# Performance work log

Measured on AMD Instinct MI355X. Metric: run time of the kernel, lower is better.

Reference implementation:

```python
import jax, jax.numpy as jnp
import numpy as np

# dims
B, C, H, W = 8, 256, 64, 128
P = 4                      # patch size (p1 == p2)
E = C // 2                 # embed dim = ngf//2 = Mamba d_model
HP, WP = H // P, W // P
N = HP * WP                # 512 tokens
DM = E                     # Mamba d_model
DI = 2 * DM                # d_inner (expand=2)
DS = 16                    # d_state
DC = 4                     # d_conv
DR = DM // 16              # dt_rank
NG = 128                   # new_ngf
S = 2                      # pixel-shuffle stride


def setup_inputs() -> dict:
    key = jax.random.key(0)
    ks = jax.random.split(key, 16)
    g = lambda i, shape, s=0.02: jax.random.normal(ks[i], shape, jnp.float32) * s
    return {
        'x': jax.random.normal(ks[0], (B, C, H, W), jnp.float32),
        # patch embed (conv k=stride=P)
        'patch_w': g(1, (E, C, P, P)),
        'patch_b': jnp.zeros((E,), jnp.float32),
        # Mamba params
        'in_proj_w': g(2, (2 * DI, DM)),
        'conv1d_w': g(3, (DI, DC), 0.1),
        'conv1d_b': jnp.zeros((DI,), jnp.float32),
        'x_proj_w': g(4, (DR + 2 * DS, DI)),
        'dt_proj_w': g(5, (DI, DR), 0.1),
        'dt_proj_b': jnp.full((DI,), -3.0, jnp.float32),
        'A_log': jnp.log(jnp.broadcast_to(jnp.arange(1, DS + 1, dtype=jnp.float32), (DI, DS))),
        'D_param': jnp.ones((DI,), jnp.float32),
        'out_proj_w': g(6, (DM, DI)),
        # unpatchify linear N -> N*P*P
        'lin_w': g(7, (N * P * P, N)),
        'lin_b': jnp.zeros((N * P * P,), jnp.float32),
        # nerv conv (3x3, out = new_ngf*S*S)
        'conv_w': g(8, (NG * S * S, E, 3, 3), 0.05),
        'conv_b': jnp.zeros((NG * S * S,), jnp.float32),
        # residual FFN (1x1)
        'ffn_w1': g(9, (NG, NG)),
        'ffn_b1': jnp.zeros((NG,), jnp.float32),
        'ffn_w2': g(10, (NG, NG)),
        'ffn_b2': jnp.zeros((NG,), jnp.float32),
    }


def reference(x, patch_w, patch_b, in_proj_w, conv1d_w, conv1d_b, x_proj_w,
              dt_proj_w, dt_proj_b, A_log, D_param, out_proj_w, lin_w, lin_b,
              conv_w, conv_b, ffn_w1, ffn_b1, ffn_w2, ffn_b2):
    silu = jax.nn.silu
    # ---- patch embed: (B,C,H,W) -> (B,N,E)
    t = jax.lax.conv_general_dilated(x, patch_w, (P, P), 'VALID',
                                     dimension_numbers=('NCHW', 'OIHW', 'NCHW'))
    t = t + patch_b[None, :, None, None]
    t = t.reshape(B, E, N).transpose(0, 2, 1)  # (B,N,E)

    # ---- Mamba selective scan
    xz = jnp.einsum('bld,ed->ble', t, in_proj_w)      # (B,N,2*DI)
    xin, z = jnp.split(xz, 2, axis=-1)
    # depthwise causal conv1d over sequence
    xp = jnp.pad(xin, ((0, 0), (DC - 1, 0), (0, 0)))
    xc = sum(xp[:, k:k + N, :] * conv1d_w[:, k] for k in range(DC)) + conv1d_b
    xc = silu(xc)                                     # (B,N,DI)
    dbl = jnp.einsum('bld,ed->ble', xc, x_proj_w)
    dt, Bs, Cs = dbl[..., :DR], dbl[..., DR:DR + DS], dbl[..., DR + DS:]
    dt = jax.nn.softplus(jnp.einsum('blr,dr->bld', dt, dt_proj_w) + dt_proj_b)
    A = -jnp.exp(A_log)                               # (DI,DS)
    dA = jnp.exp(dt[..., None] * A)                   # (B,N,DI,DS)
    dBx = dt[..., None] * Bs[:, :, None, :] * xc[..., None]

    def step(h, inputs):
        dA_t, dBx_t, C_t = inputs
        h = dA_t * h + dBx_t                          # (B,DI,DS)
        y = jnp.einsum('bdn,bn->bd', h, C_t)
        return h, y

    h0 = jnp.zeros((B, DI, DS), xc.dtype)
    _, ys = jax.lax.scan(step, h0, (dA.transpose(1, 0, 2, 3),
                                    dBx.transpose(1, 0, 2, 3),
                                    Cs.transpose(1, 0, 2)))
    y = ys.transpose(1, 0, 2) + D_param * xc
    y = y * silu(z)
    out = jnp.einsum('bld,ed->ble', y, out_proj_w)    # (B,N,DM)

    # ---- unpatchify: (B,N,E) -> (B,E,H,W)
    u = out.transpose(0, 2, 1)                        # (B,E,N)
    u = jnp.einsum('ben,mn->bem', u, lin_w) + lin_b   # (B,E,N*P*P)
    u = u.reshape(B, E, HP, WP, P, P).transpose(0, 1, 2, 4, 3, 5)
    u = u.reshape(B, E, H, W)

    # ---- nerv block: 3x3 conv -> pixel shuffle -> gelu
    c = jax.lax.conv_general_dilated(u, conv_w, (1, 1), ((1, 1), (1, 1)),
                                     dimension_numbers=('NCHW', 'OIHW', 'NCHW'))
    c = c + conv_b[None, :, None, None]               # (B,NG*S*S,H,W)
    c = c.reshape(B, NG, S, S, H, W).transpose(0, 1, 4, 2, 5, 3)
    c = c.reshape(B, NG, H * S, W * S)
    c = jax.nn.gelu(c)

    # ---- residual FFN (1x1 convs over channels)
    f = jax.nn.gelu(jnp.einsum('bchw,ec->behw', c, ffn_w1) + ffn_b1[None, :, None, None])
    f = jnp.einsum('behw,ce->bchw', f, ffn_w2) + ffn_b2[None, :, None, None]
    return c + f
```

## Files before the change

### kernel.cpp

```cpp
#include <hip/hip_runtime.h>
#include <hip/hip_bf16.h>

#define HW2 32768

typedef __attribute__((ext_vector_type(8))) short short8v;
typedef __attribute__((ext_vector_type(4))) float f32x4;

__device__ __forceinline__ float siluf(float x){ return x / (1.f + __expf(-x)); }
__device__ __forceinline__ float geluf(float v){
  float t = 0.7978845608028654f * fmaf(0.044715f*v*v, v, v);
  t = fminf(fmaxf(t, -15.f), 15.f);
  float e = __expf(2.f*t);
  return 0.5f*v*(1.f + (e-1.f)/(e+1.f));
}
__device__ __forceinline__ ushort bf16rne(float f){
  unsigned u = __float_as_uint(f);
  unsigned r = (u + 0x7fffu + ((u >> 16) & 1u)) >> 16;
  return (ushort)r;
}
__device__ __forceinline__ float bf2f(ushort u){ return __uint_as_float(((unsigned)u) << 16); }
__device__ __forceinline__ void split2(float v, ushort& h, ushort& lo){
  h = bf16rne(v);
  lo = bf16rne(v - bf2f(h));
}

__global__ __launch_bounds__(256) void k_prep(uint4* __restrict__ ubf4,
                                              const float* __restrict__ cw, ushort* __restrict__ wbf,
                                              const float* __restrict__ w1, const float* __restrict__ w2,
                                              ushort* __restrict__ wpad,
                                              const float* __restrict__ lw, ushort* __restrict__ lwbf){
  int bid = blockIdx.x;
  int tid = threadIdx.x;
  if (bid < 32) {
    uint4 z = make_uint4(0,0,0,0);
    size_t base4 = (size_t)bid * 34320;
    for (int i = tid; i < 1552; i += 256) {
      size_t off;
      if (i < 520)       off = i;
      else if (i < 1040) off = 33800 + (i - 520);
      else {
        int j = i - 1040;
        int row = 1 + (j >> 3);
        int colsel = (j >> 2) & 1, q = j & 3;
        off = (size_t)row*520 + colsel*516 + q;
      }
      ubf4[base4 + off] = z;
    }
  } else if (bid < 2336) {
    int idx = (bid - 32)*256 + tid;
    int j    = idx & 7;
    int lane = (idx >> 3) & 63;
    int f    = (idx >> 9) & 3;
    int tap  = (idx >> 11) % 9;
    int rest = idx / 18432;
    int ec = rest & 3, ocg = rest >> 2;
    int o = ocg*64 + f*16 + (lane & 15);
    int e = ec*32 + (lane >> 4)*8 + j;
    wbf[idx] = bf16rne(cw[((size_t)o*128 + e)*9 + tap]);
  } else if (bid < 2472) {
    int idx = (bid - 2336)*256 + tid;
    int which = idx / 17408;
    int rem = idx - which*17408;
    int e = rem / 136, k = rem - e*136;
    const float* s = which ? w2 : w1;
    wpad[idx] = (k < 128) ? bf16rne(s[e*128 + k]) : (ushort)0;
  } else {
    int i = (bid - 2472)*256 + tid;
    float4 v = reinterpret_cast<const float4*>(lw)[i];
    uint2 u;
    u.x = (uint)bf16rne(v.x) | ((uint)bf16rne(v.y) << 16);
    u.y = (uint)bf16rne(v.z) | ((uint)bf16rne(v.w) << 16);
    reinterpret_cast<uint2*>(lwbf)[i] = u;
  }
}

__global__ __launch_bounds__(256) void k_ytr(const float* __restrict__ yo, ushort* __restrict__ ybfT){
  __shared__ float tile[32][132];
  int b = blockIdx.x, n0 = blockIdx.y*32;
  int tid = threadIdx.x;
  for (int it = 0; it < 16; ++it) {
    int idx = it*256 + tid;
    int row = idx >> 7, e = idx & 127;
    tile[row][e] = yo[((size_t)(b*512 + n0 + row))*128 + e];
  }
  __syncthreads();
  int e = tid >> 1, half = tid & 1;
  uint* dst = reinterpret_cast<uint*>(ybfT + ((size_t)b*128 + e)*512 + n0 + half*16);
  #pragma unroll
  for (int j = 0; j < 8; ++j) {
    int n = half*16 + j*2;
    dst[j] = (uint)bf16rne(tile[n][e]) | ((uint)bf16rne(tile[n+1][e]) << 16);
  }
}

__global__ __launch_bounds__(256) void k_patchm(const float* __restrict__ x, const float* __restrict__ pw,
                                                float* __restrict__ part){
  __shared__ ushort Ah[4096], Al[4096], Wh[4096], Wl[4096];
  int m0 = blockIdx.x * 128;
  int ks = blockIdx.y;
  int tid = threadIdx.x;
  int l = tid & 63, wv = tid >> 6;
  int wm = wv >> 1, we = wv & 1;
  int lj = l & 15, lg = l >> 4;
  f32x4 acc[4][4];
  #pragma unroll
  for (int a = 0; a < 4; ++a)
    #pragma unroll
    for (int b = 0; b < 4; ++b)
      acc[a][b] = (f32x4){0.f,0.f,0.f,0.f};
  int kbase = ks * 256;

  for (int it = 0; it < 8; ++it) {
    int k0 = kbase + it*32;
    __syncthreads();
    #pragma unroll
    for (int q = 0; q < 4; ++q) {
      int flat = q*256 + tid;
      int row = flat & 127, kk4 = flat >> 7;
      int m = m0 + row;
      int bb = m >> 9, ll = m & 511;
      int hp = ll >> 5, wp = ll & 31;
      int k = k0 + kk4*4;
      int c = k >> 4, i2 = (k >> 2) & 3;
      float4 v = *reinterpret_cast<const float4*>(x + (((bb*256 + c)*64 + hp*4 + i2)*128 + wp*4));
      ushort h0,h1,h2,h3,q0,q1,q2,q3;
      split2(v.x,h0,q0); split2(v.y,h1,q1); split2(v.z,h2,q2); split2(v.w,h3,q3);
      uint2 uh, ul;
      uh.x = (uint)h0 | ((uint)h1 << 16); uh.y = (uint)h2 | ((uint)h3 << 16);
      ul.x = (uint)q0 | ((uint)q1 << 16); ul.y = (uint)q2 | ((uint)q3 << 16);
      int lane = ((kk4 >> 1) << 4) | (row & 15);
      int dst = ((row >> 4)*64 + lane)*8 + (kk4 & 1)*4;
      *reinterpret_cast<uint2*>(Ah + dst) = uh;
      *reinterpret_cast<uint2*>(Al + dst) = ul;
    }
    #pragma unroll
    for (int q = 0; q < 4; ++q) {
      int flat = q*256 + tid;
      int e = flat >> 3, kk4 = flat & 7;
      float4 v = *reinterpret_cast<const float4*>(pw + (size_t)e*4096 + k0 + kk4*4);
      ushort h0,h1,h2,h3,q0,q1,q2,q3;
      split2(v.x,h0,q0); split2(v.y,h1,q1); split2(v.z,h2,q2); split2(v.w,h3,q3);
      uint2 uh, ul;
      uh.x = (uint)h0 | ((uint)h1 << 16); uh.y = (uint)h2 | ((uint)h3 << 16);
      ul.x = (uint)q0 | ((uint)q1 << 16); ul.y = (uint)q2 | ((uint)q3 << 16);
      int lane = ((kk4 >> 1) << 4) | (e & 15);
      int dst = ((e >> 4)*64 + lane)*8 + (kk4 & 1)*4;
      *reinterpret_cast<uint2*>(Wh + dst) = uh;
      *reinterpret_cast<uint2*>(Wl + dst) = ul;
    }
    __syncthreads();

    short8v ah[4], al_[4], wh[4], wl_[4];
    #pragma unroll
    for (int f = 0; f < 4; ++f) {
      ah[f]  = *reinterpret_cast<const short8v*>(Ah + ((wm*4 + f)*64 + l)*8);
      al_[f] = *reinterpret_cast<const short8v*>(Al + ((wm*4 + f)*64 + l)*8);
      wh[f]  = *reinterpret_cast<const short8v*>(Wh + ((we*4 + f)*64 + l)*8);
      wl_[f] = *reinterpret_cast<const short8v*>(Wl + ((we*4 + f)*64 + l)*8);
    }
    #pragma unroll
    for (int fo = 0; fo < 4; ++fo)
      #pragma unroll
      for (int fj = 0; fj < 4; ++fj) {
        acc[fo][fj] = __builtin_amdgcn_mfma_f32_16x16x32_bf16(ah[fo],  wh[fj],  acc[fo][fj], 0, 0, 0);
        acc[fo][fj] = __builtin_amdgcn_mfma_f32_16x16x32_bf16(ah[fo],  wl_[fj], acc[fo][fj], 0, 0, 0);
        acc[fo][fj] = __builtin_amdgcn_mfma_f32_16x16x32_bf16(al_[fo], wh[fj],  acc[fo][fj], 0, 0, 0);
      }
  }
  float* pb = part + (size_t)ks*524288;
  #pragma unroll
  for (int fo = 0; fo < 4; ++fo) {
    int m = m0 + wm*64 + fo*16 + lg*4;
    #pragma unroll
    for (int fj = 0; fj < 4; ++fj) {
      int e = we*64 + fj*16 + lj;
      f32x4 a = acc[fo][fj];
      pb[(size_t)(m+0)*128 + e] = a.x;
      pb[(size_t)(m+1)*128 + e] = a.y;
      pb[(size_t)(m+2)*128 + e] = a.z;
      pb[(size_t)(m+3)*128 + e] = a.w;
    }
  }
}

__global__ __launch_bounds__(256) void k_tred(const float* __restrict__ part, const float* __restrict__ pb,
                                              float* __restrict__ t){
  int i = blockIdx.x*256 + threadIdx.x;
  const float4* p4 = reinterpret_cast<const float4*>(part);
  float4 s = reinterpret_cast<const float4*>(pb)[i & 31];
  #pragma unroll
  for (int ks = 0; ks < 16; ++ks) {
    float4 v = p4[(size_t)ks*131072 + i];
    s.x += v.x; s.y += v.y; s.z += v.z; s.w += v.w;
  }
  reinterpret_cast<float4*>(t)[i] = s;
}

__global__ __launch_bounds__(256) void k_gemm(const float* __restrict__ A, const float* __restrict__ W,
                                              float* __restrict__ C, int M, int N, int K){
  __shared__ __align__(16) float As[16][68];
  __shared__ __align__(16) float Bs[16][68];
  int m0 = blockIdx.x * 64, n0 = blockIdx.y * 64;
  int tid = threadIdx.x;
  int tm = tid >> 4, tn = tid & 15;
  int lm = tid >> 2, kq = tid & 3;
  float acc[4][4] = {};
  const float* Abase = A + (size_t)(m0 + lm)*K + kq*4;
  const float* Wbase = W + (size_t)(n0 + lm)*K + kq*4;
  for (int k0 = 0; k0 < K; k0 += 16) {
    float4 av = *reinterpret_cast<const float4*>(Abase + k0);
    float4 bv = *reinterpret_cast<const float4*>(Wbase + k0);
    As[kq*4+0][lm]=av.x; As[kq*4+1][lm]=av.y; As[kq*4+2][lm]=av.z; As[kq*4+3][lm]=av.w;
    Bs[kq*4+0][lm]=bv.x; Bs[kq*4+1][lm]=bv.y; Bs[kq*4+2][lm]=bv.z; Bs[kq*4+3][lm]=bv.w;
    __syncthreads();
    #pragma unroll
    for (int kk = 0; kk < 16; ++kk) {
      float4 a = *reinterpret_cast<const float4*>(&As[kk][tm*4]);
      float4 b = *reinterpret_cast<const float4*>(&Bs[kk][tn*4]);
      float ar[4] = {a.x,a.y,a.z,a.w};
      float br[4] = {b.x,b.y,b.z,b.w};
      #pragma unroll
      for (int i = 0; i < 4; ++i)
        #pragma unroll
        for (int j = 0; j < 4; ++j)
          acc[i][j] = fmaf(ar[i], br[j], acc[i][j]);
    }
    __syncthreads();
  }
  #pragma unroll
  for (int i = 0; i < 4; ++i) {
    float4 ov = make_float4(acc[i][0], acc[i][1], acc[i][2], acc[i][3]);
    *reinterpret_cast<float4*>(C + (size_t)(m0 + tm*4 + i)*N + n0 + tn*4) = ov;
  }
}

__global__ __launch_bounds__(256) void k_conv1d(const float* __restrict__ xz, const float* __restrict__ w,
                                                const float* __restrict__ bias, float* __restrict__ xc){
  int idx = blockIdx.x*256 + threadIdx.x;
  int d = idx & 255;
  int l = (idx >> 8) & 511;
  int bb = idx >> 17;
  const float* base = xz + (size_t)bb*512*512 + d;
  float s = bias[d];
  #pragma unroll
  for (int k = 0; k < 4; ++k) {
    int ls = l - 3 + k;
    if (ls >= 0) s = fmaf(base[(size_t)ls*512], w[d*4+k], s);
  }
  xc[idx] = s / (1.f + __expf(-s));
}

__global__ __launch_bounds__(256) void k_xproj(const float* __restrict__ xc, const float* __restrict__ xpw,
                                               const float* __restrict__ dtw, const float* __restrict__ dtb,
                                               float* __restrict__ dbl, float* __restrict__ dt){
  __shared__ __align__(16) float sxc[256];
  __shared__ float sdbl[40];
  int bl = blockIdx.x;
  int tid = threadIdx.x;
  sxc[tid] = xc[(size_t)bl*256 + tid];
  __syncthreads();
  if (tid < 160) {
    int g = tid >> 2, kq = tid & 3;
    const float4* wr = reinterpret_cast<const float4*>(xpw + g*256) + kq;
    const float4* xr = reinterpret_cast<const float4*>(sxc) + kq;
    float s = 0.f;
    #pragma unroll
    for (int i = 0; i < 16; ++i) {
      float4 w = wr[i*4], xv = xr[i*4];
      s += w.x*xv.x + w.y*xv.y + w.z*xv.z + w.w*xv.w;
    }
    s += __shfl_xor(s, 1);
    s += __shfl_xor(s, 2);
    if (kq == 0) {
      sdbl[g] = s;
      dbl[(size_t)bl*40 + g] = s;
    }
  }
  __syncthreads();
  float s = dtb[tid];
  const float* wr = dtw + tid*8;
  #pragma unroll
  for (int r = 0; r < 8; ++r) s = fmaf(sdbl[r], wr[r], s);
  float sp = (s > 20.f) ? s : log1pf(__expf(s));
  dt[(size_t)bl*256 + tid] = sp;
}

__global__ __launch_bounds__(256) void k_scanA(const float* __restrict__ dt, const float* __restrict__ dbl,
                                               const float* __restrict__ xc, const float* __restrict__ A_log,
                                               float* __restrict__ aprod, float* __restrict__ hend){
  __shared__ float sdt[32][16], sxc[32][16], sB[32][16];
  int tid = threadIdx.x;
  int bg = blockIdx.x;
  int ch = blockIdx.y;
  int bb = bg >> 4, dgrp = bg & 15;
  int l0 = ch*32;
  #pragma unroll
  for (int it = 0; it < 2; ++it) {
    int idx = it*256 + tid;
    int t = idx >> 4, dd = idx & 15;
    int base = bb*512 + l0 + t;
    sdt[t][dd] = dt[(size_t)base*256 + dgrp*16 + dd];
    sxc[t][dd] = xc[(size_t)base*256 + dgrp*16 + dd];
    sB [t][dd] = dbl[(size_t)base*40 + 8 + dd];
  }
  __syncthreads();
  int n = tid & 15, dloc = tid >> 4;
  float Ac = -__expf(A_log[(dgrp*16 + dloc)*16 + n]);
  float a = 1.f, h = 0.f;
  #pragma unroll
  for (int t = 0; t < 32; ++t) {
    float dtv = sdt[t][dloc], xcv = sxc[t][dloc], Bv = sB[t][n];
    float dA = __expf(dtv*Ac);
    h = fmaf(dA, h, dtv*Bv*xcv);
    a *= dA;
  }
  aprod[(size_t)(bg*16 + ch)*256 + tid] = a;
  hend [(size_t)(bg*16 + ch)*256 + tid] = h;
}

__global__ __launch_bounds__(256) void k_scanC(const float* __restrict__ dt, const float* __restrict__ dbl,
                                               const float* __restrict__ xc, const float* __restrict__ xz,
                                               const float* __restrict__ A_log, const float* __restrict__ Dp,
                                               const float* __restrict__ aprod, const float* __restrict__ hend,
                                               float* __restrict__ y){
  __shared__ float sdt[32][16], sxc[32][16], sB[32][16], sC[32][16], sz[32][16];
  int tid = threadIdx.x;
  int bg = blockIdx.x;
  int ch = blockIdx.y;
  int bb = bg >> 4, dgrp = bg & 15;
  int l0 = ch*32;
  #pragma unroll
  for (int it = 0; it < 2; ++it) {
    int idx = it*256 + tid;
    int t = idx >> 4, dd = idx & 15;
    int base = bb*512 + l0 + t;
    sdt[t][dd] = dt[(size_t)base*256 + dgrp*16 + dd];
    sxc[t][dd] = xc[(size_t)base*256 + dgrp*16 + dd];
    sB [t][dd] = dbl[(size_t)base*40 + 8  + dd];
    sC [t][dd] = dbl[(size_t)base*40 + 24 + dd];
    sz [t][dd] = xz[(size_t)base*512 + 256 + dgrp*16 + dd];
  }
  float h = 0.f;
  for (int cc = 0; cc < ch; ++cc) {
    size_t idx = (size_t)(bg*16 + cc)*256 + tid;
    h = fmaf(aprod[idx], h, hend[idx]);
  }
  __syncthreads();
  int n = tid & 15, dloc = tid >> 4;
  int d = dgrp*16 + dloc;
  float Ac = -__expf(A_log[d*16 + n]);
  float Dv = Dp[d];
  #pragma unroll 4
  for (int t = 0; t < 32; ++t) {
    float dtv = sdt[t][dloc], xcv = sxc[t][dloc];
    float Bv = sB[t][n], Cv = sC[t][n];
    float dA = __expf(dtv*Ac);
    h = fmaf(dA, h, dtv*Bv*xcv);
    float yp = h*Cv;
    yp += __shfl_xor(yp, 1, 16);
    yp += __shfl_xor(yp, 2, 16);
    yp += __shfl_xor(yp, 4, 16);
    yp += __shfl_xor(yp, 8, 16);
    if (n == 0) {
      float zv = sz[t][dloc];
      y[(size_t)(bb*512 + l0 + t)*256 + d] = (yp + Dv*xcv) * (zv / (1.f + __expf(-zv)));
    }
  }
}

__global__ __launch_bounds__(512) void k_linm(const ushort* __restrict__ ybfT, const ushort* __restrict__ lwbf,
                                              const float* __restrict__ lb, ushort* __restrict__ ubf){
  __shared__ ushort As[128*88];
  __shared__ ushort Bs[128*88];
  int m0 = blockIdx.x * 128;
  int b  = blockIdx.y;
  int tid = threadIdx.x;
  int l = tid & 63, wv = tid >> 6;
  int wm = wv & 3, we = wv >> 2;
  int lj = l & 15, lg = l >> 4;
  f32x4 acc[4][2];
  #pragma unroll
  for (int fo = 0; fo < 4; ++fo)
    #pragma unroll
    for (int fj = 0; fj < 2; ++fj)
      acc[fo][fj] = (f32x4){0.f,0.f,0.f,0.f};

  for (int k0 = 0; k0 < 512; k0 += 64) {
    __syncthreads();
    #pragma unroll
    for (int it = 0; it < 2; ++it) {
      int flat = it*512 + tid;
      int e = flat >> 3, kc8 = flat & 7;
      *reinterpret_cast<uint4*>(&As[e*88 + kc8*8]) =
        *reinterpret_cast<const uint4*>(ybfT + ((size_t)b*128 + e)*512 + k0 + kc8*8);
      *reinterpret_cast<uint4*>(&Bs[e*88 + kc8*8]) =
        *reinterpret_cast<const uint4*>(lwbf + (size_t)(m0 + e)*512 + k0 + kc8*8);
    }
    __syncthreads();
    #pragma unroll
    for (int kc = 0; kc < 2; ++kc) {
      short8v af[4], bq[2];
      #pragma unroll
      for (int fo = 0; fo < 4; ++fo)
        af[fo] = *reinterpret_cast<const short8v*>(&As[(we*64 + fo*16 + lj)*88 + kc*32 + lg*8]);
      #pragma unroll
      for (int fj = 0; fj < 2; ++fj)
        bq[fj] = *reinterpret_cast<const short8v*>(&Bs[(wm*32 + fj*16 + lj)*88 + kc*32 + lg*8]);
      #pragma unroll
      for (int fo = 0; fo < 4; ++fo)
        #pragma unroll
        for (int fj = 0; fj < 2; ++fj)
          acc[fo][fj] = __builtin_amdgcn_mfma_f32_16x16x32_bf16(af[fo], bq[fj], acc[fo][fj], 0, 0, 0);
    }
  }
  #pragma unroll
  for (int fj = 0; fj < 2; ++fj) {
    int m = m0 + wm*32 + fj*16 + lj;
    float bias = lb[m];
    int hh = ((m >> 9) << 2) + ((m >> 2) & 3);
    int ww = (((m >> 4) & 31) << 2) + (m & 3);
    #pragma unroll
    for (int fo = 0; fo < 4; ++fo) {
      int eg = we*2 + (fo >> 1);
      int e5 = ((fo & 1) << 4) + (lg << 2);
      f32x4 a = acc[fo][fj];
      uint2 u;
      u.x = (uint)bf16rne(a.x + bias) | ((uint)bf16rne(a.y + bias) << 16);
      u.y = (uint)bf16rne(a.z + bias) | ((uint)bf16rne(a.w + bias) << 16);
      *reinterpret_cast<uint2*>(ubf + ((((size_t)b*4 + eg)*66 + hh + 1)*130 + ww + 1)*32 + e5) = u;
    }
  }
}

__global__ __launch_bounds__(512, 4) void k_conv3m(const ushort* __restrict__ ubf, const ushort* __restrict__ wbf,
                                                   const float* __restrict__ cb, ushort* __restrict__ cbf){
  __shared__ ushort wlds[36864];
  int h2 = blockIdx.x;
  int bz = blockIdx.y;
  int bb = bz >> 2, op = bz & 3;
  int tid = threadIdx.x;
  int l   = tid & 63;
  int wv  = tid >> 6;
  int hr  = wv >> 2;
  int wseg = (wv & 3) * 32;
  int lj = l & 15, lg = l >> 4;

  f32x4 acc[8][2];
  #pragma unroll
  for (int i = 0; i < 8; ++i)
    #pragma unroll
    for (int j = 0; j < 2; ++j)
      acc[i][j] = (f32x4){0.f, 0.f, 0.f, 0.f};

  for (int ec = 0; ec < 4; ++ec) {
    __syncthreads();
    const uint4* s0 = reinterpret_cast<const uint4*>(wbf) + (size_t)((op*2    )*4 + ec)*2304;
    const uint4* s1 = reinterpret_cast<const uint4*>(wbf) + (size_t)((op*2 + 1)*4 + ec)*2304;
    uint4* dA = reinterpret_cast<uint4*>(wlds);
    for (int q = tid; q < 2304; q += 512) { dA[q] = s0[q]; dA[2304 + q] = s1[q]; }
    __syncthreads();

    const ushort* ub_ec = ubf + (((size_t)(bb*4 + ec)*66 + 2*h2 + hr)*130 + wseg + lj)*32 + lg*8;
    #pragma unroll
    for (int ki = 0; ki < 3; ++ki) {
      const ushort* bbase_p = ub_ec + (size_t)ki*4160;
      #pragma unroll
      for (int kj = 0; kj < 3; ++kj) {
        short8v bfr[2];
        #pragma unroll
        for (int f2 = 0; f2 < 2; ++f2)
          bfr[f2] = *reinterpret_cast<const short8v*>(bbase_p + (f2*16 + kj)*32);
        const ushort* wtap0 = wlds + (ki*3 + kj)*2048 + l*8;
        #pragma unroll
        for (int half = 0; half < 2; ++half) {
          const ushort* wtap = wtap0 + half*18432;
          short8v af[4];
          #pragma unroll
          for (int f = 0; f < 4; ++f)
            af[f] = *reinterpret_cast<const short8v*>(wtap + f*512);
          #pragma unroll
          for (int fo = 0; fo < 4; ++fo)
            #pragma unroll
            for (int fj = 0; fj < 2; ++fj)
              acc[half*4 + fo][fj] = __builtin_amdgcn_mfma_f32_16x16x32_bf16(af[fo], bfr[fj], acc[half*4 + fo][fj], 0, 0, 0);
        }
      }
    }
  }

  int row = h2*2 + hr;
  #pragma unroll
  for (int fo = 0; fo < 8; ++fo) {
    int obase = op*128 + fo*16 + lg*4;
    int g = obase >> 2;
    float b0 = cb[obase], b1 = cb[obase+1], b2 = cb[obase+2], b3 = cb[obase+3];
    size_t rbase0 = (((size_t)bb*128 + g)*128 + 2*row)*256;
    size_t rbase1 = rbase0 + 256;
    #pragma unroll
    for (int fj = 0; fj < 2; ++fj) {
      int w = wseg + fj*16 + lj;
      f32x4 a = acc[fo][fj];
      uint u0 = (uint)bf16rne(geluf(a.x + b0)) | ((uint)bf16rne(geluf(a.y + b1)) << 16);
      uint u1 = (uint)bf16rne(geluf(a.z + b2)) | ((uint)bf16rne(geluf(a.w + b3)) << 16);
      *reinterpret_cast<uint*>(cbf + rbase0 + 2*w) = u0;
      *reinterpret_cast<uint*>(cbf + rbase1 + 2*w) = u1;
    }
  }
}

__global__ __launch_bounds__(512) void k_ffnm(const ushort* __restrict__ wpad, const float* __restrict__ b1,
                                              const float* __restrict__ b2, const ushort* __restrict__ cbf,
                                              float* __restrict__ out){
  extern __shared__ ushort sm[];
  ushort* cT = sm;
  ushort* wl = sm + 128*136;
  int pix0 = blockIdx.x * 128;
  int bb = pix0 >> 15;
  int hw0 = pix0 & 32767;
  int tid = threadIdx.x;
  int l = tid & 63, wv = tid >> 6;
  int wc = wv >> 2, wp = wv & 3;
  int lj = l & 15, lg = l >> 4;
  int r = tid & 1, hpair = tid >> 1;
  const ushort* cbase = cbf + (size_t)bb*128*HW2 + hw0;

  for (int it = 0; it < 16; ++it) {
    int flat = it*256 + hpair;
    int pp = flat & 63;
    int cpair = flat >> 6;
    int ch = cpair*2 + r;
    uint own = *reinterpret_cast<const uint*>(cbase + (size_t)ch*HW2 + pp*2);
    uint other = __shfl_xor((int)own, 1);
    uint o = r ? ((other >> 16) | (own & 0xffff0000u))
               : ((own & 0xffffu) | (other << 16));
    *reinterpret_cast<uint*>(&cT[(pp*2 + r)*136 + cpair*2]) = o;
  }
  {
    const uint4* src = reinterpret_cast<const uint4*>(wpad);
    uint4* dst = reinterpret_cast<uint4*>(wl);
    for (int i = tid; i < 2176; i += 512) dst[i] = src[i];
  }
  __syncthreads();

  f32x4 acc[4][2];
  #pragma unroll
  for (int fo = 0; fo < 4; ++fo)
    #pragma unroll
    for (int fj = 0; fj < 2; ++fj)
      acc[fo][fj] = (f32x4){0.f,0.f,0.f,0.f};

  #pragma unroll
  for (int kc = 0; kc < 4; ++kc) {
    short8v af[4], bq[2];
    #pragma unroll
    for (int fo = 0; fo < 4; ++fo)
      af[fo] = *reinterpret_cast<const short8v*>(&wl[(wc*64 + fo*16 + lj)*136 + kc*32 + lg*8]);
    #pragma unroll
    for (int fj = 0; fj < 2; ++fj)
      bq[fj] = *reinterpret_cast<const short8v*>(&cT[(wp*32 + fj*16 + lj)*136 + kc*32 + lg*8]);
    #pragma unroll
    for (int fo = 0; fo < 4; ++fo)
      #pragma unroll
      for (int fj = 0; fj < 2; ++fj)
        acc[fo][fj] = __builtin_amdgcn_mfma_f32_16x16x32_bf16(af[fo], bq[fj], acc[fo][fj], 0, 0, 0);
  }
  __syncthreads();

  const ushort* w2g = wpad + 17408;
  short8v a2[4], a2n[4];
  #pragma unroll
  for (int fo = 0; fo < 4; ++fo)
    a2[fo] = *reinterpret_cast<const short8v*>(w2g + (size_t)(wc*64 + fo*16 + lj)*136 + lg*8);

  #pragma unroll
  for (int fo = 0; fo < 4; ++fo) {
    int ch0 = wc*64 + fo*16 + lg*4;
    float c0 = b1[ch0], c1 = b1[ch0+1], c2 = b1[ch0+2], c3 = b1[ch0+3];
    #pragma unroll
    for (int fj = 0; fj < 2; ++fj) {
      int px = wp*32 + fj*16 + lj;
      f32x4 a = acc[fo][fj];
      uint2 u;
      u.x = (uint)bf16rne(geluf(a.x + c0)) | ((uint)bf16rne(geluf(a.y + c1)) << 16);
      u.y = (uint)bf16rne(geluf(a.z + c2)) | ((uint)bf16rne(geluf(a.w + c3)) << 16);
      *reinterpret_cast<uint2*>(&wl[px*136 + ch0]) = u;
    }
  }
  __syncthreads();

  #pragma unroll
  for (int fo = 0; fo < 4; ++fo)
    #pragma unroll
    for (int fj = 0; fj < 2; ++fj)
      acc[fo][fj] = (f32x4){0.f,0.f,0.f,0.f};

  #pragma unroll
  for (int kc = 0; kc < 4; ++kc) {
    if (kc < 3) {
      #pragma unroll
      for (int fo = 0; fo < 4; ++fo)
        a2n[fo] = *reinterpret_cast<const short8v*>(w2g + (size_t)(wc*64 + fo*16 + lj)*136 + (kc+1)*32 + lg*8);
    }
    short8v bq[2];
    #pragma unroll
    for (int fj = 0; fj < 2; ++fj)
      bq[fj] = *reinterpret_cast<const short8v*>(&wl[(wp*32 + fj*16 + lj)*136 + kc*32 + lg*8]);
    #pragma unroll
    for (int fo = 0; fo < 4; ++fo)
      #pragma unroll
      for (int fj = 0; fj < 2; ++fj)
        acc[fo][fj] = __builtin_amdgcn_mfma_f32_16x16x32_bf16(a2[fo], bq[fj], acc[fo][fj], 0, 0, 0);
    #pragma unroll
    for (int fo = 0; fo < 4; ++fo) a2[fo] = a2n[fo];
  }

  #pragma unroll
  for (int fo = 0; fo < 4; ++fo) {
    int ch0 = wc*64 + fo*16 + lg*4;
    float d0 = b2[ch0], d1 = b2[ch0+1], d2 = b2[ch0+2], d3 = b2[ch0+3];
    #pragma unroll
    for (int fj = 0; fj < 2; ++fj) {
      int px = wp*32 + fj*16 + lj;
      f32x4 a = acc[fo][fj];
      uint2 cu = *reinterpret_cast<const uint2*>(&cT[px*136 + ch0]);
      float cv0 = __uint_as_float((cu.x & 0xffffu) << 16);
      float cv1 = __uint_as_float(cu.x & 0xffff0000u);
      float cv2 = __uint_as_float((cu.y & 0xffffu) << 16);
      float cv3 = __uint_as_float(cu.y & 0xffff0000u);
      float* p0 = out + (size_t)bb*128*HW2 + (size_t)ch0*HW2 + hw0 + px;
      p0[0]             = cv0 + a.x + d0;
      p0[HW2]           = cv1 + a.y + d1;
      p0[2*HW2]         = cv2 + a.z + d2;
      p0[3*(size_t)HW2] = cv3 + a.w + d3;
    }
  }
}

extern "C" void kernel_launch(void* const* d_in, const int* in_sizes, int n_in,
                              void* d_out, int out_size, void* d_ws, size_t ws_size,
                              hipStream_t stream) {
  const float* x          = (const float*)d_in[0];
  const float* patch_w    = (const float*)d_in[1];
  const float* patch_b    = (const float*)d_in[2];
  const float* in_proj_w  = (const float*)d_in[3];
  const float* conv1d_w   = (const float*)d_in[4];
  const float* conv1d_b   = (const float*)d_in[5];
  const float* x_proj_w   = (const float*)d_in[6];
  const float* dt_proj_w  = (const float*)d_in[7];
  const float* dt_proj_b  = (const float*)d_in[8];
  const float* A_log      = (const float*)d_in[9];
  const float* D_param    = (const float*)d_in[10];
  const float* out_proj_w = (const float*)d_in[11];
  const float* lin_w      = (const float*)d_in[12];
  const float* lin_b      = (const float*)d_in[13];
  const float* conv_w     = (const float*)d_in[14];
  const float* conv_b     = (const float*)d_in[15];
  const float* ffn_w1     = (const float*)d_in[16];
  const float* ffn_b1     = (const float*)d_in[17];
  const float* ffn_w2     = (const float*)d_in[18];
  const float* ffn_b2     = (const float*)d_in[19];
  float* out = (float*)d_out;

  ushort* ubf  = (ushort*)d_ws;
  ushort* wbf  = ubf + 10982400;
  ushort* wpad = wbf + 589824;
  float* t    = (float*)(wpad + 34816);
  float* xz   = t    + 524288;
  float* xc   = xz   + 2097152;
  float* dbl  = xc   + 1048576;
  float* dt   = dbl  + 163840;
  float* y    = dt   + 1048576;
  float* yo   = y    + 1048576;
  float* apr  = yo   + 524288;
  float* hend = apr  + 524288;
  ushort* lwbf = (ushort*)(hend + 524288);
  ushort* ybfT = lwbf + 4194304;
  ushort* cbf  = ybfT + 524288;
  float* part = (float*)(cbf + 33554432);

  k_prep  <<<dim3(6568), dim3(256), 0, stream>>>((uint4*)ubf, conv_w, wbf, ffn_w1, ffn_w2, wpad, lin_w, lwbf);
  k_patchm<<<dim3(32, 16), dim3(256), 0, stream>>>(x, patch_w, part);
  k_tred  <<<dim3(512), dim3(256), 0, stream>>>(part, patch_b, t);
  k_gemm  <<<dim3(64, 8), dim3(256), 0, stream>>>(t, in_proj_w, xz, 4096, 512, 128);
  k_conv1d<<<dim3(4096), dim3(256), 0, stream>>>(xz, conv1d_w, conv1d_b, xc);
  k_xproj <<<dim3(4096), dim3(256), 0, stream>>>(xc, x_proj_w, dt_proj_w, dt_proj_b, dbl, dt);
  k_scanA <<<dim3(128, 16), dim3(256), 0, stream>>>(dt, dbl, xc, A_log, apr, hend);
  k_scanC <<<dim3(128, 16), dim3(256), 0, stream>>>(dt, dbl, xc, xz, A_log, D_param, apr, hend, y);
  k_gemm  <<<dim3(64, 2), dim3(256), 0, stream>>>(y, out_proj_w, yo, 4096, 128, 256);
  k_ytr   <<<dim3(8, 16), dim3(256), 0, stream>>>(yo, ybfT);
  k_linm  <<<dim3(64, 8), dim3(512), 0, stream>>>(ybfT, lwbf, lin_b, ubf);
  k_conv3m<<<dim3(32, 32), dim3(512), 0, stream>>>(ubf, wbf, conv_b, cbf);
  k_ffnm  <<<dim3(2048), dim3(512), (size_t)(2*128*136)*sizeof(ushort), stream>>>(wpad, ffn_b1, ffn_b2, cbf, out);
}
```

Baseline: 307.9 us.

## Use split-bf16 MFMA for in_proj, fuse conv1d into x_proj, prefetch conv3 operands

Replaces the FP32 SIMT in_proj GEMM with an MFMA kernel that splits each float into high and low bf16 halves and accumulates three products, which keeps near-FP32 accuracy while using matrix cores. The depthwise conv1d+SiLU is folded into the x_proj/dt kernel, removing one launch and a round trip of xc through memory. In the 3x3 conv kernel all B fragments are preloaded into registers before the MFMA loop, and the occupancy hint drops from 4 to 2 blocks per CU to make room for them. This adds register pressure and lowers occupancy in the conv.

```diff
diff --git a/kernel.cpp b/kernel.cpp
--- a/kernel.cpp
+++ b/kernel.cpp
@@ -196,92 +196,133 @@
   reinterpret_cast<float4*>(t)[i] = s;
 }
 
-__global__ __launch_bounds__(256) void k_gemm(const float* __restrict__ A, const float* __restrict__ W,
-                                              float* __restrict__ C, int M, int N, int K){
-  __shared__ __align__(16) float As[16][68];
-  __shared__ __align__(16) float Bs[16][68];
-  int m0 = blockIdx.x * 64, n0 = blockIdx.y * 64;
-  int tid = threadIdx.x;
-  int tm = tid >> 4, tn = tid & 15;
-  int lm = tid >> 2, kq = tid & 3;
-  float acc[4][4] = {};
-  const float* Abase = A + (size_t)(m0 + lm)*K + kq*4;
-  const float* Wbase = W + (size_t)(n0 + lm)*K + kq*4;
-  for (int k0 = 0; k0 < K; k0 += 16) {
-    float4 av = *reinterpret_cast<const float4*>(Abase + k0);
-    float4 bv = *reinterpret_cast<const float4*>(Wbase + k0);
-    As[kq*4+0][lm]=av.x; As[kq*4+1][lm]=av.y; As[kq*4+2][lm]=av.z; As[kq*4+3][lm]=av.w;
-    Bs[kq*4+0][lm]=bv.x; Bs[kq*4+1][lm]=bv.y; Bs[kq*4+2][lm]=bv.z; Bs[kq*4+3][lm]=bv.w;
-    __syncthreads();
-    #pragma unroll
-    for (int kk = 0; kk < 16; ++kk) {
-      float4 a = *reinterpret_cast<const float4*>(&As[kk][tm*4]);
-      float4 b = *reinterpret_cast<const float4*>(&Bs[kk][tn*4]);
-      float ar[4] = {a.x,a.y,a.z,a.w};
-      float br[4] = {b.x,b.y,b.z,b.w};
-      #pragma unroll
-      for (int i = 0; i < 4; ++i)
-        #pragma unroll
-        for (int j = 0; j < 4; ++j)
-          acc[i][j] = fmaf(ar[i], br[j], acc[i][j]);
-    }
-    __syncthreads();
-  }
-  #pragma unroll
-  for (int i = 0; i < 4; ++i) {
-    float4 ov = make_float4(acc[i][0], acc[i][1], acc[i][2], acc[i][3]);
-    *reinterpret_cast<float4*>(C + (size_t)(m0 + tm*4 + i)*N + n0 + tn*4) = ov;
-  }
-}
-
-__global__ __launch_bounds__(256) void k_conv1d(const float* __restrict__ xz, const float* __restrict__ w,
-                                                const float* __restrict__ bias, float* __restrict__ xc){
-  int idx = blockIdx.x*256 + threadIdx.x;
-  int d = idx & 255;
-  int l = (idx >> 8) & 511;
-  int bb = idx >> 17;
-  const float* base = xz + (size_t)bb*512*512 + d;
-  float s = bias[d];
-  #pragma unroll
-  for (int k = 0; k < 4; ++k) {
-    int ls = l - 3 + k;
-    if (ls >= 0) s = fmaf(base[(size_t)ls*512], w[d*4+k], s);
-  }
-  xc[idx] = s / (1.f + __expf(-s));
-}
-
-__global__ __launch_bounds__(256) void k_xproj(const float* __restrict__ xc, const float* __restrict__ xpw,
-                                               const float* __restrict__ dtw, const float* __restrict__ dtb,
-                                               float* __restrict__ dbl, float* __restrict__ dt){
+__global__ __launch_bounds__(256) void k_iproj(const float* __restrict__ t, const float* __restrict__ W,
+                                               float* __restrict__ xz){
+  __shared__ ushort Ah[4096], Al[4096], Wh[4096], Wl[4096];
+  int m0 = blockIdx.x * 128;
+  int n0 = blockIdx.y * 128;
+  int tid = threadIdx.x;
+  int l = tid & 63, wv = tid >> 6;
+  int wm = wv >> 1, we = wv & 1;
+  int lj = l & 15, lg = l >> 4;
+  f32x4 acc[4][4];
+  #pragma unroll
+  for (int a = 0; a < 4; ++a)
+    #pragma unroll
+    for (int b = 0; b < 4; ++b)
+      acc[a][b] = (f32x4){0.f,0.f,0.f,0.f};
+
+  for (int it = 0; it < 4; ++it) {
+    int k0 = it*32;
+    __syncthreads();
+    #pragma unroll
+    for (int q = 0; q < 4; ++q) {
+      int flat = q*256 + tid;
+      int row = flat & 127, kk4 = flat >> 7;
+      float4 v = *reinterpret_cast<const float4*>(t + (size_t)(m0 + row)*128 + k0 + kk4*4);
+      ushort h0,h1,h2,h3,q0,q1,q2,q3;
+      split2(v.x,h0,q0); split2(v.y,h1,q1); split2(v.z,h2,q2); split2(v.w,h3,q3);
+      uint2 uh, ul;
+      uh.x = (uint)h0 | ((uint)h1 << 16); uh.y = (uint)h2 | ((uint)h3 << 16);
+      ul.x = (uint)q0 | ((uint)q1 << 16); ul.y = (uint)q2 | ((uint)q3 << 16);
+      int lane = ((kk4 >> 1) << 4) | (row & 15);
+      int dst = ((row >> 4)*64 + lane)*8 + (kk4 & 1)*4;
+      *reinterpret_cast<uint2*>(Ah + dst) = uh;
+      *reinterpret_cast<uint2*>(Al + dst) = ul;
+    }
+    #pragma unroll
+    for (int q = 0; q < 4; ++q) {
+      int flat = q*256 + tid;
+      int e = flat >> 3, kk4 = flat & 7;
+      float4 v = *reinterpret_cast<const float4*>(W + (size_t)(n0 + e)*128 + k0 + (kk4 & 7)*4);
+      ushort h0,h1,h2,h3,q0,q1,q2,q3;
+      split2(v.x,h0,q0); split2(v.y,h1,q1); split2(v.z,h2,q2); split2(v.w,h3,q3);
+      uint2 uh, ul;
+      uh.x = (uint)h0 | ((uint)h1 << 16); uh.y = (uint)h2 | ((uint)h3 << 16);
+      ul.x = (uint)q0 | ((uint)q1 << 16); ul.y = (uint)q2 | ((uint)q3 << 16);
+      int lane = ((kk4 >> 1) << 4) | (e & 15);
+      int dst = ((e >> 4)*64 + lane)*8 + (kk4 & 1)*4;
+      *reinterpret_cast<uint2*>(Wh + dst) = uh;
+      *reinterpret_cast<uint2*>(Wl + dst) = ul;
+    }
+    __syncthreads();
+
+    short8v ah[4], al_[4], wh[4], wl_[4];
+    #pragma unroll
+    for (int f = 0; f < 4; ++f) {
+      ah[f]  = *reinterpret_cast<const short8v*>(Ah + ((wm*4 + f)*64 + l)*8);
+      al_[f] = *reinterpret_cast<const short8v*>(Al + ((wm*4 + f)*64 + l)*8);
+      wh[f]  = *reinterpret_cast<const short8v*>(Wh + ((we*4 + f)*64 + l)*8);
+      wl_[f] = *reinterpret_cast<const short8v*>(Wl + ((we*4 + f)*64 + l)*8);
+    }
+    #pragma unroll
+    for (int fo = 0; fo < 4; ++fo)
+      #pragma unroll
+      for (int fj = 0; fj < 4; ++fj) {
+        acc[fo][fj] = __builtin_amdgcn_mfma_f32_16x16x32_bf16(ah[fo],  wh[fj],  acc[fo][fj], 0, 0, 0);
+        acc[fo][fj] = __builtin_amdgcn_mfma_f32_16x16x32_bf16(ah[fo],  wl_[fj], acc[fo][fj], 0, 0, 0);
+        acc[fo][fj] = __builtin_amdgcn_mfma_f32_16x16x32_bf16(al_[fo], wh[fj],  acc[fo][fj], 0, 0, 0);
+      }
+  }
+  #pragma unroll
+  for (int fo = 0; fo < 4; ++fo) {
+    int m = m0 + wm*64 + fo*16 + lg*4;
+    #pragma unroll
+    for (int fj = 0; fj < 4; ++fj) {
+      int n = n0 + we*64 + fj*16 + lj;
+      f32x4 a = acc[fo][fj];
+      xz[(size_t)(m+0)*512 + n] = a.x;
+      xz[(size_t)(m+1)*512 + n] = a.y;
+      xz[(size_t)(m+2)*512 + n] = a.z;
+      xz[(size_t)(m+3)*512 + n] = a.w;
+    }
+  }
+}
+
+__global__ __launch_bounds__(256) void k_cxp(const float* __restrict__ xz, const float* __restrict__ w1d,
+                                             const float* __restrict__ c1b,
+                                             const float* __restrict__ xpw,
+                                             const float* __restrict__ dtw, const float* __restrict__ dtb,
+                                             float* __restrict__ xc, float* __restrict__ dbl,
+                                             float* __restrict__ dt){
   __shared__ __align__(16) float sxc[256];
   __shared__ float sdbl[40];
   int bl = blockIdx.x;
-  int tid = threadIdx.x;
-  sxc[tid] = xc[(size_t)bl*256 + tid];
+  int bb = bl >> 9, ll = bl & 511;
+  int tid = threadIdx.x;
+  float s = c1b[tid];
+  #pragma unroll
+  for (int k = 0; k < 4; ++k) {
+    int ls = ll - 3 + k;
+    if (ls >= 0) s = fmaf(xz[((size_t)(bb*512 + ls))*512 + tid], w1d[tid*4 + k], s);
+  }
+  float xcv = s / (1.f + __expf(-s));
+  xc[(size_t)bl*256 + tid] = xcv;
+  sxc[tid] = xcv;
   __syncthreads();
   if (tid < 160) {
     int g = tid >> 2, kq = tid & 3;
     const float4* wr = reinterpret_cast<const float4*>(xpw + g*256) + kq;
     const float4* xr = reinterpret_cast<const float4*>(sxc) + kq;
-    float s = 0.f;
+    float sv = 0.f;
     #pragma unroll
     for (int i = 0; i < 16; ++i) {
       float4 w = wr[i*4], xv = xr[i*4];
-      s += w.x*xv.x + w.y*xv.y + w.z*xv.z + w.w*xv.w;
-    }
-    s += __shfl_xor(s, 1);
-    s += __shfl_xor(s, 2);
+      sv += w.x*xv.x + w.y*xv.y + w.z*xv.z + w.w*xv.w;
+    }
+    sv += __shfl_xor(sv, 1);
+    sv += __shfl_xor(sv, 2);
     if (kq == 0) {
-      sdbl[g] = s;
-      dbl[(size_t)bl*40 + g] = s;
+      sdbl[g] = sv;
+      dbl[(size_t)bl*40 + g] = sv;
     }
   }
   __syncthreads();
-  float s = dtb[tid];
+  float sd = dtb[tid];
   const float* wr = dtw + tid*8;
   #pragma unroll
-  for (int r = 0; r < 8; ++r) s = fmaf(sdbl[r], wr[r], s);
-  float sp = (s > 20.f) ? s : log1pf(__expf(s));
+  for (int r = 0; r < 8; ++r) sd = fmaf(sdbl[r], wr[r], sd);
+  float sp = (sd > 20.f) ? sd : log1pf(__expf(sd));
   dt[(size_t)bl*256 + tid] = sp;
 }
 
@@ -368,6 +409,44 @@
   }
 }
 
+__global__ __launch_bounds__(256) void k_gemm(const float* __restrict__ A, const float* __restrict__ W,
+                                              float* __restrict__ C, int M, int N, int K){
+  __shared__ __align__(16) float As[16][68];
+  __shared__ __align__(16) float Bs[16][68];
+  int m0 = blockIdx.x * 64, n0 = blockIdx.y * 64;
+  int tid = threadIdx.x;
+  int tm = tid >> 4, tn = tid & 15;
+  int lm = tid >> 2, kq = tid & 3;
+  float acc[4][4] = {};
+  const float* Abase = A + (size_t)(m0 + lm)*K + kq*4;
+  const float* Wbase = W + (size_t)(n0 + lm)*K + kq*4;
+  for (int k0 = 0; k0 < K; k0 += 16) {
+    float4 av = *reinterpret_cast<const float4*>(Abase + k0);
+    float4 bv = *reinterpret_cast<const float4*>(Wbase + k0);
+    As[kq*4+0][lm]=av.x; As[kq*4+1][lm]=av.y; As[kq*4+2][lm]=av.z; As[kq*4+3][lm]=av.w;
+    Bs[kq*4+0][lm]=bv.x; Bs[kq*4+1][lm]=bv.y; Bs[kq*4+2][lm]=bv.z; Bs[kq*4+3][lm]=bv.w;
+    __syncthreads();
+    #pragma unroll
+    for (int kk = 0; kk < 16; ++kk) {
+      float4 a = *reinterpret_cast<const float4*>(&As[kk][tm*4]);
+      float4 b = *reinterpret_cast<const float4*>(&Bs[kk][tn*4]);
+      float ar[4] = {a.x,a.y,a.z,a.w};
+      float br[4] = {b.x,b.y,b.z,b.w};
+      #pragma unroll
+      for (int i = 0; i < 4; ++i)
+        #pragma unroll
+        for (int j = 0; j < 4; ++j)
+          acc[i][j] = fmaf(ar[i], br[j], acc[i][j]);
+    }
+    __syncthreads();
+  }
+  #pragma unroll
+  for (int i = 0; i < 4; ++i) {
+    float4 ov = make_float4(acc[i][0], acc[i][1], acc[i][2], acc[i][3]);
+    *reinterpret_cast<float4*>(C + (size_t)(m0 + tm*4 + i)*N + n0 + tn*4) = ov;
+  }
+}
+
 __global__ __launch_bounds__(512) void k_linm(const ushort* __restrict__ ybfT, const ushort* __restrict__ lwbf,
                                               const float* __restrict__ lb, ushort* __restrict__ ubf){
   __shared__ ushort As[128*88];
@@ -432,7 +511,7 @@
   }
 }
 
-__global__ __launch_bounds__(512, 4) void k_conv3m(const ushort* __restrict__ ubf, const ushort* __restrict__ wbf,
+__global__ __launch_bounds__(512, 2) void k_conv3m(const ushort* __restrict__ ubf, const ushort* __restrict__ wbf,
                                                    const float* __restrict__ cb, ushort* __restrict__ cbf){
   __shared__ ushort wlds[36864];
   int h2 = blockIdx.x;
@@ -461,15 +540,19 @@
     __syncthreads();
 
     const ushort* ub_ec = ubf + (((size_t)(bb*4 + ec)*66 + 2*h2 + hr)*130 + wseg + lj)*32 + lg*8;
+    short8v bfr[3][2][3];
+    #pragma unroll
+    for (int ki = 0; ki < 3; ++ki)
+      #pragma unroll
+      for (int f2 = 0; f2 < 2; ++f2)
+        #pragma unroll
+        for (int kj = 0; kj < 3; ++kj)
+          bfr[ki][f2][kj] = *reinterpret_cast<const short8v*>(ub_ec + (size_t)ki*4160 + (f2*16 + kj)*32);
+
     #pragma unroll
     for (int ki = 0; ki < 3; ++ki) {
-      const ushort* bbase_p = ub_ec + (size_t)ki*4160;
       #pragma unroll
       for (int kj = 0; kj < 3; ++kj) {
-        short8v bfr[2];
-        #pragma unroll
-        for (int f2 = 0; f2 < 2; ++f2)
-          bfr[f2] = *reinterpret_cast<const short8v*>(bbase_p + (f2*16 + kj)*32);
         const ushort* wtap0 = wlds + (ki*3 + kj)*2048 + l*8;
         #pragma unroll
         for (int half = 0; half < 2; ++half) {
@@ -482,7 +565,7 @@
           for (int fo = 0; fo < 4; ++fo)
             #pragma unroll
             for (int fj = 0; fj < 2; ++fj)
-              acc[half*4 + fo][fj] = __builtin_amdgcn_mfma_f32_16x16x32_bf16(af[fo], bfr[fj], acc[half*4 + fo][fj], 0, 0, 0);
+              acc[half*4 + fo][fj] = __builtin_amdgcn_mfma_f32_16x16x32_bf16(af[fo], bfr[ki][fj][kj], acc[half*4 + fo][fj], 0, 0, 0);
         }
       }
     }
@@ -681,9 +764,8 @@
   k_prep  <<<dim3(6568), dim3(256), 0, stream>>>((uint4*)ubf, conv_w, wbf, ffn_w1, ffn_w2, wpad, lin_w, lwbf);
   k_patchm<<<dim3(32, 16), dim3(256), 0, stream>>>(x, patch_w, part);
   k_tred  <<<dim3(512), dim3(256), 0, stream>>>(part, patch_b, t);
-  k_gemm  <<<dim3(64, 8), dim3(256), 0, stream>>>(t, in_proj_w, xz, 4096, 512, 128);
-  k_conv1d<<<dim3(4096), dim3(256), 0, stream>>>(xz, conv1d_w, conv1d_b, xc);
-  k_xproj <<<dim3(4096), dim3(256), 0, stream>>>(xc, x_proj_w, dt_proj_w, dt_proj_b, dbl, dt);
+  k_iproj <<<dim3(32, 4), dim3(256), 0, stream>>>(t, in_proj_w, xz);
+  k_cxp   <<<dim3(4096), dim3(256), 0, stream>>>(xz, conv1d_w, conv1d_b, x_proj_w, dt_proj_w, dt_proj_b, xc, dbl, dt);
   k_scanA <<<dim3(128, 16), dim3(256), 0, stream>>>(dt, dbl, xc, A_log, apr, hend);
   k_scanC <<<dim3(128, 16), dim3(256), 0, stream>>>(dt, dbl, xc, xz, A_log, D_param, apr, hend, y);
   k_gemm  <<<dim3(64, 2), dim3(256), 0, stream>>>(y, out_proj_w, yo, 4096, 128, 256);
```

New measurement: 304.1 us. About the same (-1.2%).
